# Optimization experiments

Hardware: AMD Instinct MI355X
Metric: run time of the kernel (lower is better)

## Reference

```python
import jax, jax.numpy as jnp
import numpy as np

CHEB_K = 3
HIDDEN = 64
HORIZON = 12
OUT_DIM = 1


def _supports(E, K):
    # adaptive adjacency: softmax(relu(E E^T)) rows, Chebyshev polynomial stack [K, N, N]
    A = jax.nn.softmax(jax.nn.relu(E @ E.T), axis=1)
    N = E.shape[0]
    s = [jnp.eye(N, dtype=E.dtype), A]
    for _ in range(2, K):
        s.append(2.0 * (A @ s[-1]) - s[-2])
    return jnp.stack(s, axis=0)


def _gconv(x, supports, W, b):
    # x: [B,N,C], supports: [K,N,N], W: [N,K,C,O], b: [N,O] -> [B,N,O]
    xg = jnp.einsum('knm,bmc->bnkc', supports, x)
    return jnp.einsum('bnkc,nkco->bno', xg, W) + b


def _agcrn_layer(x_seq, supports, gW, gb, uW, ub):
    # x_seq: [B,T,N,C]; returns full hidden sequence [B,T,N,H]
    B, T, N, _ = x_seq.shape
    h0 = jnp.zeros((B, N, HIDDEN), dtype=x_seq.dtype)

    def step(h, x):
        zr = jax.nn.sigmoid(_gconv(jnp.concatenate([x, h], axis=-1), supports, gW, gb))
        z, r = zr[..., :HIDDEN], zr[..., HIDDEN:]
        hc = jnp.tanh(_gconv(jnp.concatenate([x, z * h], axis=-1), supports, uW, ub))
        h_new = r * h + (1.0 - r) * hc
        return h_new, h_new

    _, hs = jax.lax.scan(step, h0, jnp.swapaxes(x_seq, 0, 1))  # [T,B,N,H]
    return jnp.swapaxes(hs, 0, 1)


def _forward(source, E, pools, conv_w, conv_b):
    supports = _supports(E, CHEB_K)
    cur = source
    for (gwp, gbp, uwp, ubp) in pools:
        # per-node weights from embedding pool (hoisted: E is constant over time)
        gW = jnp.einsum('nd,dkio->nkio', E, gwp)
        gb = E @ gbp
        uW = jnp.einsum('nd,dkio->nkio', E, uwp)
        ub = E @ ubp
        cur = _agcrn_layer(cur, supports, gW, gb, uW, ub)
    last = cur[:, -1]  # [B,N,H]
    # end_conv: Conv2d(1, horizon*out_dim, kernel=(1,H)) == linear over H per node
    y = jnp.einsum('bnh,oh->bon', last, conv_w) + conv_b[None, :, None]  # [B, horizon*out, N]
    B, _, N = y.shape
    y = y.reshape(B, HORIZON, OUT_DIM, N).transpose(0, 1, 3, 2)  # [B, horizon, N, out_dim]
    return y


def setup_inputs() -> dict:
    key = jax.random.key(0)
    ks = jax.random.split(key, 12)
    B, T, N, C, D, H = 64, 12, 2000, 1, 16, HIDDEN
    s = 0.1  # keep gates/tanh unsaturated
    return {
        'source': jax.random.normal(ks[0], (B, T, N, C), jnp.float32),
        'node_embeddings': jax.random.normal(ks[1], (N, D), jnp.float32),
        'gate_wpool_0': jax.random.normal(ks[2], (D, CHEB_K, C + H, 2 * H), jnp.float32) * s,
        'gate_bpool_0': jax.random.normal(ks[3], (D, 2 * H), jnp.float32) * s,
        'update_wpool_0': jax.random.normal(ks[4], (D, CHEB_K, C + H, H), jnp.float32) * s,
        'update_bpool_0': jax.random.normal(ks[5], (D, H), jnp.float32) * s,
        'gate_wpool_1': jax.random.normal(ks[6], (D, CHEB_K, 2 * H, 2 * H), jnp.float32) * s,
        'gate_bpool_1': jax.random.normal(ks[7], (D, 2 * H), jnp.float32) * s,
        'update_wpool_1': jax.random.normal(ks[8], (D, CHEB_K, 2 * H, H), jnp.float32) * s,
        'update_bpool_1': jax.random.normal(ks[9], (D, H), jnp.float32) * s,
        'conv_w': jax.random.normal(ks[10], (HORIZON * OUT_DIM, H), jnp.float32) * s,
        'conv_b': jax.random.normal(ks[11], (HORIZON * OUT_DIM,), jnp.float32) * s,
    }


def reference(source, node_embeddings, gate_wpool_0, gate_bpool_0, update_wpool_0,
              update_bpool_0, gate_wpool_1, gate_bpool_1, update_wpool_1,
              update_bpool_1, conv_w, conv_b):
    pools = [
        (gate_wpool_0, gate_bpool_0, update_wpool_0, update_bpool_0),
        (gate_wpool_1, gate_bpool_1, update_wpool_1, update_bpool_1),
    ]
    return _forward(source, node_embeddings, pools, conv_w, conv_b)
```

## Files before the change

### kernel.cpp

```cpp
#include <hip/hip_runtime.h>
#include <hip/hip_bf16.h>
#include <math.h>

#define NN 2000
#define DD 16
#define BB 64
#define TT 12
#define HH 64
#define MR 4000
#define SCL 2048.0f
#define ISCL (1.0f / 2048.0f)

typedef _Float16 f16;
typedef __attribute__((ext_vector_type(8))) _Float16 frag8h;
typedef __attribute__((ext_vector_type(4))) float floatx4;

__device__ inline float fin(float v) {
  return (v == v && v > -1e30f && v < 1e30f) ? v : 0.f;
}
__device__ inline float sigmoid_safe(float x) {
  float e = expf(-fabsf(x));
  float s = 1.f / (1.f + e);
  return x >= 0.f ? s : 1.f - s;
}
__device__ inline float tanh_safe(float x) {
  float e = expf(-2.f * fabsf(x));
  float r = (1.f - e) / (1.f + e);
  return x >= 0.f ? r : -r;
}
__device__ inline void split16(float v, f16& hi, f16& lo) {
  hi = (f16)v;
  lo = (f16)((v - (float)hi) * SCL);
}
__device__ inline void gll16(const void* g, void* l) {
  __builtin_amdgcn_global_load_lds((const __attribute__((address_space(1))) void*)g,
                                   (__attribute__((address_space(3))) void*)l, 16, 0, 0);
}

__global__ void kzero(float* p, int n) {
  int i = blockIdx.x * 256 + threadIdx.x;
  if (i < n) p[i] = 0.f;
}

__global__ __launch_bounds__(256) void ka(const float* __restrict__ E,
                                          float* __restrict__ A) {
  __shared__ float s[NN];
  __shared__ float red[256];
  int n = blockIdx.x;
  float en[DD];
#pragma unroll
  for (int d = 0; d < DD; ++d) en[d] = fin(E[n * DD + d]);
  float lmax = 0.f;
  for (int m = threadIdx.x; m < NN; m += 256) {
    float acc = 0.f;
#pragma unroll
    for (int d = 0; d < DD; ++d) acc += en[d] * fin(E[m * DD + d]);
    acc = fmaxf(acc, 0.f);
    s[m] = acc;
    lmax = fmaxf(lmax, acc);
  }
  red[threadIdx.x] = lmax;
  __syncthreads();
  for (int w = 128; w > 0; w >>= 1) {
    if (threadIdx.x < w) red[threadIdx.x] = fmaxf(red[threadIdx.x], red[threadIdx.x + w]);
    __syncthreads();
  }
  float mx = red[0];
  __syncthreads();
  float lsum = 0.f;
  for (int m = threadIdx.x; m < NN; m += 256) {
    float e = expf(s[m] - mx);
    s[m] = e;
    lsum += e;
  }
  red[threadIdx.x] = lsum;
  __syncthreads();
  for (int w = 128; w > 0; w >>= 1) {
    if (threadIdx.x < w) red[threadIdx.x] += red[threadIdx.x + w];
    __syncthreads();
  }
  float inv = 1.f / red[0];
  for (int m = threadIdx.x; m < NN; m += 256) A[(size_t)n * NN + m] = s[m] * inv;
}

#define TM 64
#define TK 32
__global__ __launch_bounds__(256) void kg(const float* __restrict__ A,
                                          const float* __restrict__ V,
                                          float* __restrict__ C, int cols) {
  __shared__ float As[TK][TM + 1];
  __shared__ float Bs[TK][TM + 1];
  int r0 = blockIdx.x * TM;
  int c0 = blockIdx.y * TM;
  int tid = threadIdx.x;
  int tx = tid % 16;
  int ty = tid / 16;
  float acc[4][4];
#pragma unroll
  for (int i = 0; i < 4; ++i)
#pragma unroll
    for (int j = 0; j < 4; ++j) acc[i][j] = 0.f;
  for (int k0 = 0; k0 < NN; k0 += TK) {
    for (int i = tid; i < TM * TK; i += 256) {
      int rr = i / TK, kk = i % TK;
      int gr = r0 + rr, gk = k0 + kk;
      As[kk][rr] = (gr < NN && gk < NN) ? A[(size_t)gr * NN + gk] : 0.f;
    }
    for (int i = tid; i < TK * TM; i += 256) {
      int kk = i / TM, cc = i % TM;
      int gk = k0 + kk, gc = c0 + cc;
      Bs[kk][cc] = (gk < NN && gc < cols) ? V[(size_t)gk * cols + gc] : 0.f;
    }
    __syncthreads();
#pragma unroll 4
    for (int kk = 0; kk < TK; ++kk) {
      float a[4], b[4];
#pragma unroll
      for (int i = 0; i < 4; ++i) a[i] = As[kk][ty * 4 + i];
#pragma unroll
      for (int j = 0; j < 4; ++j) b[j] = Bs[kk][tx * 4 + j];
#pragma unroll
      for (int i = 0; i < 4; ++i)
#pragma unroll
        for (int j = 0; j < 4; ++j) acc[i][j] += a[i] * b[j];
    }
    __syncthreads();
  }
#pragma unroll
  for (int i = 0; i < 4; ++i) {
    int gr = r0 + ty * 4 + i;
    if (gr >= NN) continue;
#pragma unroll
    for (int j = 0; j < 4; ++j) {
      int gc = c0 + tx * 4 + j;
      if (gc < cols) C[(size_t)gr * cols + gc] = acc[i][j];
    }
  }
}

__global__ void ksplitM(const float* __restrict__ A, const float* __restrict__ A2,
                        f16* __restrict__ Mh, f16* __restrict__ Ml) {
  int i = blockIdx.x * 256 + threadIdx.x;
  if (i >= MR * NN) return;
  int m = i / NN;
  int k = i % NN;
  float v;
  if (m < NN) v = A[(size_t)m * NN + k];
  else {
    int mm = m - NN;
    v = 2.f * A2[(size_t)mm * NN + k] - (mm == k ? 1.f : 0.f);
  }
  f16 hi, lo;
  split16(v, hi, lo);
  Mh[i] = hi;
  Ml[i] = lo;
}

__global__ __launch_bounds__(256) void kconvT(const float* __restrict__ V,
                                              f16* __restrict__ Th,
                                              f16* __restrict__ Tl, int cols) {
  __shared__ float sh[32][33];
  int k0 = blockIdx.x * 32;
  int c0 = blockIdx.y * 32;
  int tx = threadIdx.x % 32;
  int ty = threadIdx.x / 32;
#pragma unroll
  for (int i = 0; i < 4; ++i) {
    int r = k0 + ty + i * 8;
    int c = c0 + tx;
    sh[ty + i * 8][tx] = (r < NN && c < cols) ? V[(size_t)r * cols + c] : 0.f;
  }
  __syncthreads();
#pragma unroll
  for (int i = 0; i < 4; ++i) {
    int cc = c0 + ty + i * 8;
    int kk = k0 + tx;
    if (cc < cols && kk < NN) {
      f16 hi, lo;
      split16(sh[tx][ty + i * 8], hi, lo);
      Th[(size_t)cc * NN + kk] = hi;
      Tl[(size_t)cc * NN + kk] = lo;
    }
  }
}

#define KT 32
__global__ __launch_bounds__(256, 2) void kmm(const f16* __restrict__ Mh,
                                              const f16* __restrict__ Ml,
                                              const f16* __restrict__ Bh,
                                              const f16* __restrict__ Bl,
                                              float* __restrict__ C1,
                                              float* __restrict__ C2, int cols) {
  __shared__ __align__(16) f16 Ash[128 * KT];
  __shared__ __align__(16) f16 Asl[128 * KT];
  __shared__ __align__(16) f16 Bsh[128 * KT];
  __shared__ __align__(16) f16 Bsl[128 * KT];
  int tid = threadIdx.x;
  int lane = tid & 63;
  int wave = tid >> 6;
  int wr = wave >> 1;
  int wc = wave & 1;
  int gx = gridDim.x;
  int nwg = gx * gridDim.y;
  int wg = blockIdx.y * gx + blockIdx.x;
  int q = nwg >> 3, r = nwg & 7;
  int xcd = wg & 7, lid = wg >> 3;
  int swz = (xcd < r ? xcd * (q + 1) : r * (q + 1) + (xcd - r) * q) + lid;
  int bx = swz % gx;
  int by = swz / gx;
  floatx4 acc0[4][4], acc1[4][4];
#pragma unroll
  for (int i = 0; i < 4; ++i)
#pragma unroll
    for (int j = 0; j < 4; ++j) {
      acc0[i][j] = (floatx4){0.f, 0.f, 0.f, 0.f};
      acc1[i][j] = (floatx4){0.f, 0.f, 0.f, 0.f};
    }
  const frag8h zf = {0, 0, 0, 0, 0, 0, 0, 0};

  auto comp = [&]() {
    frag8h ah[4], al[4], bh[4], bl[4];
#pragma unroll
    for (int mi = 0; mi < 4; ++mi) {
      int jr = wr * 4 + mi;
      ah[mi] = *(const frag8h*)(&Ash[jr * 512 + lane * 8]);
      al[mi] = *(const frag8h*)(&Asl[jr * 512 + lane * 8]);
    }
#pragma unroll
    for (int ni = 0; ni < 4; ++ni) {
      int jc = wc * 4 + ni;
      bh[ni] = *(const frag8h*)(&Bsh[jc * 512 + lane * 8]);
      bl[ni] = *(const frag8h*)(&Bsl[jc * 512 + lane * 8]);
    }
#pragma unroll
    for (int mi = 0; mi < 4; ++mi)
#pragma unroll
      for (int ni = 0; ni < 4; ++ni) {
        acc0[mi][ni] = __builtin_amdgcn_mfma_f32_16x16x32_f16(ah[mi], bh[ni], acc0[mi][ni], 0, 0, 0);
        acc1[mi][ni] = __builtin_amdgcn_mfma_f32_16x16x32_f16(ah[mi], bl[ni], acc1[mi][ni], 0, 0, 0);
        acc1[mi][ni] = __builtin_amdgcn_mfma_f32_16x16x32_f16(al[mi], bh[ni], acc1[mi][ni], 0, 0, 0);
      }
  };

  const int lr = lane & 15;
  const int lq = lane >> 4;
  for (int k0 = 0; k0 + KT <= NN; k0 += KT) {
#pragma unroll
    for (int jj = 0; jj < 2; ++jj) {
      int j = wave * 2 + jj;
      int r2 = j * 16 + lr;
      size_t ko = (size_t)k0 + lq * 8;
      int gra = bx * 128 + r2;
      if (gra < MR) {
        gll16(Mh + (size_t)gra * NN + ko, Ash + j * 512);
        gll16(Ml + (size_t)gra * NN + ko, Asl + j * 512);
      }
      int grb = by * 128 + r2;
      if (grb < cols) {
        gll16(Bh + (size_t)grb * NN + ko, Bsh + j * 512);
        gll16(Bl + (size_t)grb * NN + ko, Bsl + j * 512);
      }
    }
    __syncthreads();
    comp();
    __syncthreads();
  }
  {
    int k0 = (NN / KT) * KT;
    if (k0 < NN) {
      for (int c = tid; c < 512; c += 256) {
        int j = c >> 6;
        int ll = c & 63;
        int qq = ll >> 4;
        int rr = ll & 15;
        int r2 = j * 16 + rr;
        int gk = k0 + qq * 8;
        bool kok = (gk + 8 <= NN);
        int gra = bx * 128 + r2;
        bool aok = kok && (gra < MR);
        size_t ga = (size_t)gra * NN + gk;
        *(frag8h*)(&Ash[c * 8]) = aok ? *(const frag8h*)(Mh + ga) : zf;
        *(frag8h*)(&Asl[c * 8]) = aok ? *(const frag8h*)(Ml + ga) : zf;
        int grb = by * 128 + r2;
        bool bok = kok && (grb < cols);
        size_t gb = (size_t)grb * NN + gk;
        *(frag8h*)(&Bsh[c * 8]) = bok ? *(const frag8h*)(Bh + gb) : zf;
        *(frag8h*)(&Bsl[c * 8]) = bok ? *(const frag8h*)(Bl + gb) : zf;
      }
      __syncthreads();
      comp();
      __syncthreads();
    }
  }
#pragma unroll
  for (int mi = 0; mi < 4; ++mi) {
#pragma unroll
    for (int ni = 0; ni < 4; ++ni) {
#pragma unroll
      for (int reg = 0; reg < 4; ++reg) {
        int row = bx * 128 + wr * 64 + mi * 16 + (lane >> 4) * 4 + reg;
        int col = by * 128 + wc * 64 + ni * 16 + (lane & 15);
        if (col >= cols || row >= MR) continue;
        float v = acc0[mi][ni][reg] + acc1[mi][ni][reg] * ISCL;
        if (row < NN) C1[(size_t)row * cols + col] = v;
        else C2[(size_t)(row - NN) * cols + col] = v;
      }
    }
  }
}

__global__ void kx(const float* __restrict__ src, float* __restrict__ xb,
                   int t, int b0, int CB) {
  int i = blockIdx.x * 256 + threadIdx.x;
  if (i >= NN * CB) return;
  int bb = i % CB;
  int n = i / CB;
  xb[i] = fin(src[((size_t)(b0 + bb) * TT + t) * NN + n]);
}

__global__ void kxa(const float* __restrict__ src, float* __restrict__ xa,
                    int b0, int CB) {
  int i = blockIdx.x * 256 + threadIdx.x;
  if (i >= NN * TT * CB) return;
  int bb = i % CB;
  int t = (i / CB) % TT;
  int n = i / (CB * TT);
  xa[i] = fin(src[((size_t)(b0 + bb) * TT + t) * NN + n]);
}

__global__ void kmulz(float* __restrict__ zb, const float* __restrict__ h, int n) {
  int i = blockIdx.x * 256 + threadIdx.x;
  if (i < n) zb[i] = zb[i] * h[i];
}

__global__ __launch_bounds__(256) void kwc(const float* __restrict__ E,
                                           const float* __restrict__ wp,
                                           int Ctot, int O, float* __restrict__ W) {
  __shared__ float esm[DD];
  int n = blockIdx.x;
  int tid = threadIdx.x;
  if (tid < DD) esm[tid] = fin(E[n * DD + tid]);
  __syncthreads();
  int total = 3 * Ctot * O;
  for (int i = tid; i < total; i += 256) {
    int o = i % O;
    int rc = i / O;
    int k = rc / Ctot;
    int crow = rc - k * Ctot;
    float wa = 0.f;
#pragma unroll
    for (int d = 0; d < DD; ++d)
      wa += esm[d] * fin(wp[((size_t)(d * 3 + k) * Ctot + crow) * O + o]);
    W[((size_t)(n * 3 + k) * Ctot + crow) * O + o] = wa;
  }
}

template <int O, int CB>
__global__ __launch_bounds__(256) void kgc(
    const float* __restrict__ x0, const float* __restrict__ x1, const float* __restrict__ x2,
    const float* __restrict__ wp, const float* __restrict__ pW,
    int Ctot, int base_c, int nC, int ldn,
    const float* __restrict__ E, const float* __restrict__ bp,
    int act, int accum, float* outA, float* outB,
    int update, const float* __restrict__ rb, float* hio) {
  __shared__ float xs[8][CB + 1];
  __shared__ float ws[8][O];
  __shared__ float esm[DD];
  int n = blockIdx.x;
  int tid = threadIdx.x;
  int to = tid % 16;
  int tb = tid / 16;
  if (tid < DD) esm[tid] = fin(E[n * DD + tid]);
  __syncthreads();
  constexpr int NO = O / 16;
  constexpr int NB = CB / 16;
  float acc[NB][NO];
#pragma unroll
  for (int i = 0; i < NB; ++i)
#pragma unroll
    for (int j = 0; j < NO; ++j) acc[i][j] = 0.f;
  const size_t nb = (size_t)n * CB;
  const size_t nx = (size_t)n * ldn;
  for (int k = 0; k < 3; ++k) {
    const float* xk = (k == 0) ? x0 : (k == 1) ? x1 : x2;
    for (int c0 = 0; c0 < nC; c0 += 8) {
      int chunk = (nC - c0 < 8) ? (nC - c0) : 8;
      for (int i = tid; i < chunk * CB; i += 256) {
        int cc = i % chunk;
        int b = i / chunk;
        xs[cc][b] = xk[nx + (size_t)b * nC + c0 + cc];
      }
      if (pW) {
        const float* wrow = pW + ((size_t)(n * 3 + k) * Ctot + base_c + c0) * O;
        for (int i = tid; i < chunk * O; i += 256) {
          int o = i % O;
          int cc = i / O;
          ws[cc][o] = wrow[(size_t)cc * O + o];
        }
      } else {
        for (int i = tid; i < chunk * O; i += 256) {
          int o = i % O;
          int cc = i / O;
          int crow = base_c + c0 + cc;
          float wa = 0.f;
#pragma unroll
          for (int d = 0; d < DD; ++d)
            wa += esm[d] * fin(wp[((size_t)(d * 3 + k) * Ctot + crow) * O + o]);
          ws[cc][o] = wa;
        }
      }
      __syncthreads();
      for (int cc = 0; cc < chunk; ++cc) {
        float xv[NB];
#pragma unroll
        for (int i = 0; i < NB; ++i) xv[i] = xs[cc][tb + 16 * i];
#pragma unroll
        for (int j = 0; j < NO; ++j) {
          float wv = ws[cc][to + 16 * j];
#pragma unroll
          for (int i = 0; i < NB; ++i) acc[i][j] += xv[i] * wv;
        }
      }
      __syncthreads();
    }
  }
#pragma unroll
  for (int i2 = 0; i2 < NB; ++i2) {
    int b = tb + 16 * i2;
#pragma unroll
    for (int j = 0; j < NO; ++j) {
      int o = to + 16 * j;
      float r = acc[i2][j];
      float* dst = (o < HH || !outB) ? (outA + (nb + b) * HH + (o % HH))
                                     : (outB + (nb + b) * HH + (o - HH));
      if (accum) r += *dst;
      if (bp) {
        float ba = 0.f;
#pragma unroll
        for (int d = 0; d < DD; ++d) ba += esm[d] * fin(bp[d * O + o]);
        r += ba;
      }
      r = fin(r);
      if (act == 1) r = sigmoid_safe(r);
      else if (act == 2) r = tanh_safe(r);
      if (update) {
        float rg = rb[(nb + b) * HH + o];
        float hold = hio[(nb + b) * HH + o];
        hio[(nb + b) * HH + o] = rg * hold + (1.f - rg) * r;
      } else {
        *dst = r;
      }
    }
  }
}

__global__ void kfin(const float* __restrict__ h1, const float* __restrict__ cw,
                     const float* __restrict__ cb, float* __restrict__ out,
                     int b0, int CB) {
  int idx = blockIdx.x * 256 + threadIdx.x;
  if (idx >= CB * TT * NN) return;
  int n = idx % NN;
  int o = (idx / NN) % TT;
  int bb = idx / (NN * TT);
  const float* hp = h1 + ((size_t)n * CB + bb) * HH;
  float acc = fin(cb[o]);
#pragma unroll
  for (int hh = 0; hh < HH; ++hh) acc += hp[hh] * fin(cw[o * HH + hh]);
  out[((size_t)(b0 + bb) * TT + o) * NN + n] = fin(acc);
}

template <int CB>
static void run_chunks(const float* src, const float* E,
                       const float* gwp0, const float* gbp0,
                       const float* uwp0, const float* ubp0,
                       const float* gwp1, const float* gbp1,
                       const float* uwp1, const float* ubp1,
                       const float* cw, const float* cb,
                       float* out, f16* Mh, f16* Ml,
                       const float* pg0, const float* pu0,
                       const float* pg1, const float* pu1,
                       char* wsp, size_t off0, bool roomy, hipStream_t stream) {
  size_t off = off0;
  auto allocf = [&](size_t nelem) {
    float* p = (float*)(wsp + off);
    off += (nelem * 4 + 255) & ~(size_t)255;
    return p;
  };
  auto alloch = [&](size_t nelem) {
    f16* p = (f16*)(wsp + off);
    off += (nelem * 2 + 255) & ~(size_t)255;
    return p;
  };
  const int C = CB * HH;
  const int XC = TT * CB;
  const size_t NC = (size_t)NN * C;
  float* P1  = allocf(NC);
  float* P2  = allocf(NC);
  float* h0  = allocf(NC);
  float* h1  = allocf(NC);
  float* zb  = allocf(NC);
  float* rbf = allocf(NC);
  float* hc  = allocf(NC);
  f16* vh = alloch(NC);
  f16* vl = alloch(NC);
  float *P1c = nullptr, *P2c = nullptr;
  float *xa = nullptr, *xb1a = nullptr, *xb2a = nullptr;
  float *xb0 = nullptr, *xb1 = nullptr, *xb2 = nullptr;
  f16 *xth, *xtl;
  if (roomy) {
    P1c = allocf(NC);
    P2c = allocf(NC);
    xa   = allocf((size_t)NN * XC);
    xb1a = allocf((size_t)NN * XC);
    xb2a = allocf((size_t)NN * XC);
    xth = alloch((size_t)NN * XC);
    xtl = alloch((size_t)NN * XC);
  } else {
    xb0 = allocf((size_t)NN * CB);
    xb1 = allocf((size_t)NN * CB);
    xb2 = allocf((size_t)NN * CB);
    xth = alloch((size_t)NN * CB);
    xtl = alloch((size_t)NN * CB);
  }

  const int EW = (int)((NC + 255) / 256);
  const dim3 gConv((NN + 31) / 32, (C + 31) / 32);
  const dim3 gMM((MR + 127) / 128, (C + 127) / 128);
  float* nul = nullptr;

  auto chain_to = [&](const float* V, float* D1, float* D2) {
    kconvT<<<gConv, 256, 0, stream>>>(V, vh, vl, C);
    kmm<<<gMM, 256, 0, stream>>>(Mh, Ml, vh, vl, D1, D2, C);
  };

  for (int b0 = 0; b0 < BB; b0 += CB) {
    kzero<<<EW, 256, 0, stream>>>(h0, (int)NC);
    kzero<<<EW, 256, 0, stream>>>(h1, (int)NC);
    if (roomy) {
      kxa<<<((NN * XC) + 255) / 256, 256, 0, stream>>>(src, xa, b0, CB);
      dim3 gcx((NN + 31) / 32, (XC + 31) / 32);
      kconvT<<<gcx, 256, 0, stream>>>(xa, xth, xtl, XC);
      dim3 gmx((MR + 127) / 128, (XC + 127) / 128);
      kmm<<<gmx, 256, 0, stream>>>(Mh, Ml, xth, xtl, xb1a, xb2a, XC);
    }
    for (int t = 0; t < TT; ++t) {
      const bool tz = (t == 0);
      const float *xt0, *xt1, *xt2;
      int xln;
      if (roomy) {
        xt0 = xa + t * CB;
        xt1 = xb1a + t * CB;
        xt2 = xb2a + t * CB;
        xln = XC;
      } else {
        kx<<<(NN * CB + 255) / 256, 256, 0, stream>>>(src, xb0, t, b0, CB);
        dim3 gcx((NN + 31) / 32, (CB + 31) / 32);
        kconvT<<<gcx, 256, 0, stream>>>(xb0, xth, xtl, CB);
        dim3 gmx((MR + 127) / 128, (CB + 127) / 128);
        kmm<<<gmx, 256, 0, stream>>>(Mh, Ml, xth, xtl, xb1, xb2, CB);
        xt0 = xb0; xt1 = xb1; xt2 = xb2;
        xln = CB;
      }
      const float *g1, *g2;
      if (tz) { g1 = h0; g2 = h0; }
      else if (roomy) { g1 = P1c; g2 = P2c; }
      else { chain_to(h0, P1, P2); g1 = P1; g2 = P2; }
      kgc<128, CB><<<NN, 256, 0, stream>>>(h0, g1, g2, gwp0, pg0, 65, 1, 64, C, E, nullptr,
                                           0, 0, zb, rbf, 0, nul, nul);
      kgc<128, CB><<<NN, 256, 0, stream>>>(xt0, xt1, xt2, gwp0, pg0, 65, 0, 1, xln, E, gbp0,
                                           1, 1, zb, rbf, 0, nul, nul);
      kgc<64, CB><<<NN, 256, 0, stream>>>(xt0, xt1, xt2, uwp0, pu0, 65, 0, 1, xln, E, nullptr,
                                          0, 0, hc, nul, 0, nul, nul);
      kmulz<<<EW, 256, 0, stream>>>(zb, h0, (int)NC);
      if (tz) {
        kgc<64, CB><<<NN, 256, 0, stream>>>(zb, zb, zb, uwp0, pu0, 65, 1, 64, C, E, ubp0,
                                            2, 1, hc, nul, 1, rbf, h0);
      } else {
        chain_to(zb, P1, P2);
        kgc<64, CB><<<NN, 256, 0, stream>>>(zb, P1, P2, uwp0, pu0, 65, 1, 64, C, E, ubp0,
                                            2, 1, hc, nul, 1, rbf, h0);
      }
      if (tz) {
        kgc<128, CB><<<NN, 256, 0, stream>>>(h1, h1, h1, gwp1, pg1, 128, 64, 64, C, E, nullptr,
                                             0, 0, zb, rbf, 0, nul, nul);
      } else {
        chain_to(h1, P1, P2);
        kgc<128, CB><<<NN, 256, 0, stream>>>(h1, P1, P2, gwp1, pg1, 128, 64, 64, C, E, nullptr,
                                             0, 0, zb, rbf, 0, nul, nul);
      }
      float* q1 = roomy ? P1c : P1;
      float* q2 = roomy ? P2c : P2;
      chain_to(h0, q1, q2);
      kgc<128, CB><<<NN, 256, 0, stream>>>(h0, q1, q2, gwp1, pg1, 128, 0, 64, C, E, gbp1,
                                           1, 1, zb, rbf, 0, nul, nul);
      kgc<64, CB><<<NN, 256, 0, stream>>>(h0, q1, q2, uwp1, pu1, 128, 0, 64, C, E, nullptr,
                                          0, 0, hc, nul, 0, nul, nul);
      kmulz<<<EW, 256, 0, stream>>>(zb, h1, (int)NC);
      if (tz) {
        kgc<64, CB><<<NN, 256, 0, stream>>>(zb, zb, zb, uwp1, pu1, 128, 64, 64, C, E, ubp1,
                                            2, 1, hc, nul, 1, rbf, h1);
      } else {
        chain_to(zb, P1, P2);
        kgc<64, CB><<<NN, 256, 0, stream>>>(zb, P1, P2, uwp1, pu1, 128, 64, 64, C, E, ubp1,
                                            2, 1, hc, nul, 1, rbf, h1);
      }
    }
    kfin<<<(CB * TT * NN + 255) / 256, 256, 0, stream>>>(h1, cw, cb, out, b0, CB);
  }
}

extern "C" void kernel_launch(void* const* d_in, const int* in_sizes, int n_in,
                              void* d_out, int out_size, void* d_ws, size_t ws_size,
                              hipStream_t stream) {
  const float* src  = (const float*)d_in[0];
  const float* E    = (const float*)d_in[1];
  const float* gwp0 = (const float*)d_in[2];
  const float* gbp0 = (const float*)d_in[3];
  const float* uwp0 = (const float*)d_in[4];
  const float* ubp0 = (const float*)d_in[5];
  const float* gwp1 = (const float*)d_in[6];
  const float* gbp1 = (const float*)d_in[7];
  const float* uwp1 = (const float*)d_in[8];
  const float* ubp1 = (const float*)d_in[9];
  const float* cw   = (const float*)d_in[10];
  const float* cb   = (const float*)d_in[11];
  float* out = (float*)d_out;
  (void)in_sizes; (void)n_in; (void)out_size;

  char* wsp = (char*)d_ws;
  size_t off = 0;
  f16* Mh = (f16*)(wsp + off); off += ((size_t)MR * NN * 2 + 255) & ~(size_t)255;
  f16* Ml = (f16*)(wsp + off); off += ((size_t)MR * NN * 2 + 255) & ~(size_t)255;

  const size_t szg1 = (size_t)NN * 3 * 128 * 128;
  const size_t szu1 = (size_t)NN * 3 * 128 * 64;
  const size_t szg0 = (size_t)NN * 3 * 65 * 128;
  const size_t szu0 = (size_t)NN * 3 * 65 * 64;
  float *pg0 = nullptr, *pu0 = nullptr, *pg1 = nullptr, *pu1 = nullptr;
  bool wantAll = ws_size >= (size_t)1350 * 1000 * 1000;
  bool wantL1  = ws_size >= (size_t)1030 * 1000 * 1000;
  if (wantAll || wantL1) {
    pg1 = (float*)(wsp + off); off += (szg1 * 4 + 255) & ~(size_t)255;
    pu1 = (float*)(wsp + off); off += (szu1 * 4 + 255) & ~(size_t)255;
    if (wantAll) {
      pg0 = (float*)(wsp + off); off += (szg0 * 4 + 255) & ~(size_t)255;
      pu0 = (float*)(wsp + off); off += (szu0 * 4 + 255) & ~(size_t)255;
    }
  }
  size_t off0 = off;
  float* A  = (float*)(wsp + off0);
  float* A2 = (float*)(wsp + off0 + (((size_t)NN * NN * 4 + 255) & ~(size_t)255));

  ka<<<NN, 256, 0, stream>>>(E, A);
  {
    dim3 g((NN + TM - 1) / TM, (NN + TM - 1) / TM);
    kg<<<g, 256, 0, stream>>>(A, A, A2, NN);
  }
  ksplitM<<<(MR * NN + 255) / 256, 256, 0, stream>>>(A, A2, Mh, Ml);
  if (pg1) {
    kwc<<<NN, 256, 0, stream>>>(E, gwp1, 128, 128, pg1);
    kwc<<<NN, 256, 0, stream>>>(E, uwp1, 128, 64, pu1);
  }
  if (pg0) {
    kwc<<<NN, 256, 0, stream>>>(E, gwp0, 65, 128, pg0);
    kwc<<<NN, 256, 0, stream>>>(E, uwp0, 65, 64, pu0);
  }

  size_t rem = ws_size > off0 ? ws_size - off0 : 0;
  if (rem >= (size_t)368 * 1000 * 1000) {
    run_chunks<64>(src, E, gwp0, gbp0, uwp0, ubp0, gwp1, gbp1, uwp1, ubp1,
                   cw, cb, out, Mh, Ml, pg0, pu0, pg1, pu1, wsp, off0, true, stream);
  } else if (rem >= (size_t)288 * 1000 * 1000) {
    run_chunks<64>(src, E, gwp0, gbp0, uwp0, ubp0, gwp1, gbp1, uwp1, ubp1,
                   cw, cb, out, Mh, Ml, pg0, pu0, pg1, pu1, wsp, off0, false, stream);
  } else if (rem >= (size_t)193 * 1000 * 1000) {
    run_chunks<32>(src, E, gwp0, gbp0, uwp0, ubp0, gwp1, gbp1, uwp1, ubp1,
                   cw, cb, out, Mh, Ml, pg0, pu0, pg1, pu1, wsp, off0, true, stream);
  } else if (rem >= (size_t)153 * 1000 * 1000) {
    run_chunks<32>(src, E, gwp0, gbp0, uwp0, ubp0, gwp1, gbp1, uwp1, ubp1,
                   cw, cb, out, Mh, Ml, pg0, pu0, pg1, pu1, wsp, off0, false, stream);
  } else if (rem >= (size_t)98 * 1000 * 1000) {
    run_chunks<16>(src, E, gwp0, gbp0, uwp0, ubp0, gwp1, gbp1, uwp1, ubp1,
                   cw, cb, out, Mh, Ml, pg0, pu0, pg1, pu1, wsp, off0, true, stream);
  } else {
    run_chunks<16>(src, E, gwp0, gbp0, uwp0, ubp0, gwp1, gbp1, uwp1, ubp1,
                   cw, cb, out, Mh, Ml, pg0, pu0, pg1, pu1, wsp, off0, false, stream);
  }
}
```

Measured before the change: 54.90 ms.

## Fuse gate and update graph-conv passes into one kernel, widen channel chunks

Adds a kgf kernel that computes the full gate conv (hidden and input parts) and the input-side update conv in a single launch. The shared input tile loaded from x/h is reused for both the gate and update weight tiles, and the partial result is no longer written to global memory and read back. The shared-memory chunk in kgc and kgf grows from 8 to 16 channels, halving the number of sync rounds. Layer 1 uses the fused path only when the roomy workspace is available. The cost is more shared memory and registers per block, which may lower occupancy.

```diff
diff --git a/kernel.cpp b/kernel.cpp
--- a/kernel.cpp
+++ b/kernel.cpp
@@ -363,8 +363,8 @@
     const float* __restrict__ E, const float* __restrict__ bp,
     int act, int accum, float* outA, float* outB,
     int update, const float* __restrict__ rb, float* hio) {
-  __shared__ float xs[8][CB + 1];
-  __shared__ float ws[8][O];
+  __shared__ float xs[16][CB + 1];
+  __shared__ float ws[16][O];
   __shared__ float esm[DD];
   int n = blockIdx.x;
   int tid = threadIdx.x;
@@ -383,8 +383,8 @@
   const size_t nx = (size_t)n * ldn;
   for (int k = 0; k < 3; ++k) {
     const float* xk = (k == 0) ? x0 : (k == 1) ? x1 : x2;
-    for (int c0 = 0; c0 < nC; c0 += 8) {
-      int chunk = (nC - c0 < 8) ? (nC - c0) : 8;
+    for (int c0 = 0; c0 < nC; c0 += 16) {
+      int chunk = (nC - c0 < 16) ? (nC - c0) : 16;
       for (int i = tid; i < chunk * CB; i += 256) {
         int cc = i % chunk;
         int b = i / chunk;
@@ -450,6 +450,179 @@
       } else {
         *dst = r;
       }
+    }
+  }
+}
+
+template <int CB>
+__global__ __launch_bounds__(256) void kgf(
+    const float* __restrict__ A0, const float* __restrict__ A1, const float* __restrict__ A2,
+    int nCA, int baseA, int ldA,
+    const float* __restrict__ B0, const float* __restrict__ B1, const float* __restrict__ B2,
+    int nCB, int baseB, int ldB,
+    const float* __restrict__ wpg, const float* __restrict__ pWg,
+    const float* __restrict__ bpg,
+    const float* __restrict__ wpu, const float* __restrict__ pWu,
+    int Ctot, const float* __restrict__ E,
+    float* __restrict__ zb, float* __restrict__ rbf, float* __restrict__ hc) {
+  __shared__ float xs[16][CB + 1];
+  __shared__ float wsg[16][128];
+  __shared__ float wsu[16][64];
+  __shared__ float esm[DD];
+  int n = blockIdx.x;
+  int tid = threadIdx.x;
+  int to = tid % 16;
+  int tb = tid / 16;
+  if (tid < DD) esm[tid] = fin(E[n * DD + tid]);
+  __syncthreads();
+  constexpr int NB = CB / 16;
+  float accg[NB][8];
+  float accu[NB][4];
+#pragma unroll
+  for (int i = 0; i < NB; ++i) {
+#pragma unroll
+    for (int j = 0; j < 8; ++j) accg[i][j] = 0.f;
+#pragma unroll
+    for (int j = 0; j < 4; ++j) accu[i][j] = 0.f;
+  }
+  const size_t nb = (size_t)n * CB;
+
+  {
+    const size_t nx = (size_t)n * ldA;
+    for (int k = 0; k < 3; ++k) {
+      const float* xk = (k == 0) ? A0 : (k == 1) ? A1 : A2;
+      for (int c0 = 0; c0 < nCA; c0 += 16) {
+        int chunk = (nCA - c0 < 16) ? (nCA - c0) : 16;
+        for (int i = tid; i < chunk * CB; i += 256) {
+          int cc = i % chunk;
+          int b = i / chunk;
+          xs[cc][b] = xk[nx + (size_t)b * nCA + c0 + cc];
+        }
+        if (pWg) {
+          const float* wrow = pWg + ((size_t)(n * 3 + k) * Ctot + baseA + c0) * 128;
+          for (int i = tid; i < chunk * 128; i += 256) {
+            int o = i % 128;
+            int cc = i / 128;
+            wsg[cc][o] = wrow[(size_t)cc * 128 + o];
+          }
+        } else {
+          for (int i = tid; i < chunk * 128; i += 256) {
+            int o = i % 128;
+            int cc = i / 128;
+            int crow = baseA + c0 + cc;
+            float wa = 0.f;
+#pragma unroll
+            for (int d = 0; d < DD; ++d)
+              wa += esm[d] * fin(wpg[((size_t)(d * 3 + k) * Ctot + crow) * 128 + o]);
+            wsg[cc][o] = wa;
+          }
+        }
+        __syncthreads();
+        for (int cc = 0; cc < chunk; ++cc) {
+          float xv[NB];
+#pragma unroll
+          for (int i = 0; i < NB; ++i) xv[i] = xs[cc][tb + 16 * i];
+#pragma unroll
+          for (int j = 0; j < 8; ++j) {
+            float wv = wsg[cc][to + 16 * j];
+#pragma unroll
+            for (int i = 0; i < NB; ++i) accg[i][j] += xv[i] * wv;
+          }
+        }
+        __syncthreads();
+      }
+    }
+  }
+  {
+    const size_t nx = (size_t)n * ldB;
+    for (int k = 0; k < 3; ++k) {
+      const float* xk = (k == 0) ? B0 : (k == 1) ? B1 : B2;
+      for (int c0 = 0; c0 < nCB; c0 += 16) {
+        int chunk = (nCB - c0 < 16) ? (nCB - c0) : 16;
+        for (int i = tid; i < chunk * CB; i += 256) {
+          int cc = i % chunk;
+          int b = i / chunk;
+          xs[cc][b] = xk[nx + (size_t)b * nCB + c0 + cc];
+        }
+        if (pWg) {
+          const float* wrow = pWg + ((size_t)(n * 3 + k) * Ctot + baseB + c0) * 128;
+          for (int i = tid; i < chunk * 128; i += 256) {
+            int o = i % 128;
+            int cc = i / 128;
+            wsg[cc][o] = wrow[(size_t)cc * 128 + o];
+          }
+        } else {
+          for (int i = tid; i < chunk * 128; i += 256) {
+            int o = i % 128;
+            int cc = i / 128;
+            int crow = baseB + c0 + cc;
+            float wa = 0.f;
+#pragma unroll
+            for (int d = 0; d < DD; ++d)
+              wa += esm[d] * fin(wpg[((size_t)(d * 3 + k) * Ctot + crow) * 128 + o]);
+            wsg[cc][o] = wa;
+          }
+        }
+        if (pWu) {
+          const float* wrow = pWu + ((size_t)(n * 3 + k) * Ctot + baseB + c0) * 64;
+          for (int i = tid; i < chunk * 64; i += 256) {
+            int o = i % 64;
+            int cc = i / 64;
+            wsu[cc][o] = wrow[(size_t)cc * 64 + o];
+          }
+        } else {
+          for (int i = tid; i < chunk * 64; i += 256) {
+            int o = i % 64;
+            int cc = i / 64;
+            int crow = baseB + c0 + cc;
+            float wa = 0.f;
+#pragma unroll
+            for (int d = 0; d < DD; ++d)
+              wa += esm[d] * fin(wpu[((size_t)(d * 3 + k) * Ctot + crow) * 64 + o]);
+            wsu[cc][o] = wa;
+          }
+        }
+        __syncthreads();
+        for (int cc = 0; cc < chunk; ++cc) {
+          float xv[NB];
+#pragma unroll
+          for (int i = 0; i < NB; ++i) xv[i] = xs[cc][tb + 16 * i];
+#pragma unroll
+          for (int j = 0; j < 8; ++j) {
+            float wv = wsg[cc][to + 16 * j];
+#pragma unroll
+            for (int i = 0; i < NB; ++i) accg[i][j] += xv[i] * wv;
+          }
+#pragma unroll
+          for (int j = 0; j < 4; ++j) {
+            float wv = wsu[cc][to + 16 * j];
+#pragma unroll
+            for (int i = 0; i < NB; ++i) accu[i][j] += xv[i] * wv;
+          }
+        }
+        __syncthreads();
+      }
+    }
+  }
+#pragma unroll
+  for (int i2 = 0; i2 < NB; ++i2) {
+    int b = tb + 16 * i2;
+#pragma unroll
+    for (int j = 0; j < 8; ++j) {
+      int o = to + 16 * j;
+      float r = accg[i2][j];
+      float ba = 0.f;
+#pragma unroll
+      for (int d = 0; d < DD; ++d) ba += esm[d] * fin(bpg[d * 128 + o]);
+      r = fin(r + ba);
+      r = sigmoid_safe(r);
+      if (o < HH) zb[(nb + b) * HH + o] = r;
+      else rbf[(nb + b) * HH + (o - HH)] = r;
+    }
+#pragma unroll
+    for (int j = 0; j < 4; ++j) {
+      int o = to + 16 * j;
+      hc[(nb + b) * HH + o] = fin(accu[i2][j]);
     }
   }
 }
@@ -565,12 +738,10 @@
       if (tz) { g1 = h0; g2 = h0; }
       else if (roomy) { g1 = P1c; g2 = P2c; }
       else { chain_to(h0, P1, P2); g1 = P1; g2 = P2; }
-      kgc<128, CB><<<NN, 256, 0, stream>>>(h0, g1, g2, gwp0, pg0, 65, 1, 64, C, E, nullptr,
-                                           0, 0, zb, rbf, 0, nul, nul);
-      kgc<128, CB><<<NN, 256, 0, stream>>>(xt0, xt1, xt2, gwp0, pg0, 65, 0, 1, xln, E, gbp0,
-                                           1, 1, zb, rbf, 0, nul, nul);
-      kgc<64, CB><<<NN, 256, 0, stream>>>(xt0, xt1, xt2, uwp0, pu0, 65, 0, 1, xln, E, nullptr,
-                                          0, 0, hc, nul, 0, nul, nul);
+      kgf<CB><<<NN, 256, 0, stream>>>(h0, g1, g2, 64, 1, C,
+                                      xt0, xt1, xt2, 1, 0, xln,
+                                      gwp0, pg0, gbp0, uwp0, pu0, 65, E,
+                                      zb, rbf, hc);
       kmulz<<<EW, 256, 0, stream>>>(zb, h0, (int)NC);
       if (tz) {
         kgc<64, CB><<<NN, 256, 0, stream>>>(zb, zb, zb, uwp0, pu0, 65, 1, 64, C, E, ubp0,
@@ -580,21 +751,30 @@
         kgc<64, CB><<<NN, 256, 0, stream>>>(zb, P1, P2, uwp0, pu0, 65, 1, 64, C, E, ubp0,
                                             2, 1, hc, nul, 1, rbf, h0);
       }
-      if (tz) {
-        kgc<128, CB><<<NN, 256, 0, stream>>>(h1, h1, h1, gwp1, pg1, 128, 64, 64, C, E, nullptr,
-                                             0, 0, zb, rbf, 0, nul, nul);
+      if (roomy) {
+        const float *a1, *a2;
+        if (tz) { a1 = h1; a2 = h1; }
+        else { chain_to(h1, P1, P2); a1 = P1; a2 = P2; }
+        chain_to(h0, P1c, P2c);
+        kgf<CB><<<NN, 256, 0, stream>>>(h1, a1, a2, 64, 64, C,
+                                        h0, P1c, P2c, 64, 0, C,
+                                        gwp1, pg1, gbp1, uwp1, pu1, 128, E,
+                                        zb, rbf, hc);
       } else {
-        chain_to(h1, P1, P2);
-        kgc<128, CB><<<NN, 256, 0, stream>>>(h1, P1, P2, gwp1, pg1, 128, 64, 64, C, E, nullptr,
-                                             0, 0, zb, rbf, 0, nul, nul);
-      }
-      float* q1 = roomy ? P1c : P1;
-      float* q2 = roomy ? P2c : P2;
-      chain_to(h0, q1, q2);
-      kgc<128, CB><<<NN, 256, 0, stream>>>(h0, q1, q2, gwp1, pg1, 128, 0, 64, C, E, gbp1,
-                                           1, 1, zb, rbf, 0, nul, nul);
-      kgc<64, CB><<<NN, 256, 0, stream>>>(h0, q1, q2, uwp1, pu1, 128, 0, 64, C, E, nullptr,
-                                          0, 0, hc, nul, 0, nul, nul);
+        if (tz) {
+          kgc<128, CB><<<NN, 256, 0, stream>>>(h1, h1, h1, gwp1, pg1, 128, 64, 64, C, E, nullptr,
+                                               0, 0, zb, rbf, 0, nul, nul);
+        } else {
+          chain_to(h1, P1, P2);
+          kgc<128, CB><<<NN, 256, 0, stream>>>(h1, P1, P2, gwp1, pg1, 128, 64, 64, C, E, nullptr,
+                                               0, 0, zb, rbf, 0, nul, nul);
+        }
+        chain_to(h0, P1, P2);
+        kgc<128, CB><<<NN, 256, 0, stream>>>(h0, P1, P2, gwp1, pg1, 128, 0, 64, C, E, gbp1,
+                                             1, 1, zb, rbf, 0, nul, nul);
+        kgc<64, CB><<<NN, 256, 0, stream>>>(h0, P1, P2, uwp1, pu1, 128, 0, 64, C, E, nullptr,
+                                            0, 0, hc, nul, 0, nul, nul);
+      }
       kmulz<<<EW, 256, 0, stream>>>(zb, h1, (int)NC);
       if (tz) {
         kgc<64, CB><<<NN, 256, 0, stream>>>(zb, zb, zb, uwp1, pu1, 128, 64, 64, C, E, ubp1,
```

After: 53.87 ms. About the same (-1.9%).
